# Kernel tuning notes

Hardware: AMD Instinct MI355X
Metric: run time of the kernel (lower is better)

The kernel has to match this reference:

```python
import jax, jax.numpy as jnp
import numpy as np

N_NODES = 100000
N_EDGES = 1600000
C_IN = 128
C_OUT = 128
BN_EPS = 1e-5


def setup_inputs() -> dict:
    key = jax.random.key(0)
    k = jax.random.split(key, 4)
    x = jax.random.normal(k[0], (N_NODES, C_IN), dtype=jnp.float32)
    edge_index = jax.random.randint(k[1], (2, N_EDGES), 0, N_NODES, dtype=jnp.int32)
    # nn.Linear params (Kaiming-uniform-ish scale)
    lim = 1.0 / np.sqrt(C_IN)
    W = jax.random.uniform(k[2], (C_IN, C_OUT), jnp.float32, -lim, lim)
    b = jnp.zeros((C_OUT,), jnp.float32)
    # BatchNorm (eval mode: running stats)
    gamma = jnp.ones((C_OUT,), jnp.float32)
    beta = jnp.zeros((C_OUT,), jnp.float32)
    running_mean = jnp.zeros((C_OUT,), jnp.float32)
    running_var = jnp.ones((C_OUT,), jnp.float32)
    return {"x": x, "edge_index": edge_index, "W": W, "b": b,
            "gamma": gamma, "beta": beta,
            "running_mean": running_mean, "running_var": running_var}


def reference(x, edge_index, W, b, gamma, beta, running_mean, running_var):
    # Linear projection: [N, C_in] @ [C_in, C_out]
    h = x @ W + b
    in_node, out_node = edge_index[0], edge_index[1]
    # gather edge features then scatter-mean onto destination nodes
    sums = jax.ops.segment_sum(h[in_node], out_node, num_segments=N_NODES)
    cnt = jax.ops.segment_sum(jnp.ones((in_node.shape[0],), h.dtype), out_node,
                              num_segments=N_NODES)
    agg = sums / jnp.maximum(cnt, 1.0)[:, None]  # mean; 0 for isolated nodes
    # BatchNorm1d (eval mode: running stats) + ReLU; dropout is identity in eval
    inv = jax.lax.rsqrt(running_var + BN_EPS)
    out = (agg - running_mean) * (inv * gamma) + beta
    return jax.nn.relu(out)
```

## Files before the change

### kernel.cpp

```cpp
#include <hip/hip_runtime.h>


#define NN 100000
#define NE 1600000
#define CC 128
#define BN_EPS 1e-5f
#define LBLK 1563
#define LSTR 136
#define NBUK 256
#define DPB 391
#define ACH 4096
#define ABLK 391
#define CAP 10240

typedef __attribute__((ext_vector_type(8))) short bf16x8;
typedef __attribute__((ext_vector_type(4))) float f32x4;

static __device__ __forceinline__ short f2bf(float f) {
  union { float f; unsigned u; } v; v.f = f;
  unsigned r = (v.u + 0x7FFF + ((v.u >> 16) & 1)) >> 16;
  return (short)r;
}
static __device__ __forceinline__ float bflo(unsigned p) {
  return __uint_as_float(p << 16);
}
static __device__ __forceinline__ float bfhi(unsigned p) {
  return __uint_as_float(p & 0xffff0000u);
}

__global__ __launch_bounds__(256) void prep_zero(
    const float* __restrict__ W, const float* __restrict__ bias,
    const float* __restrict__ gamma, const float* __restrict__ beta,
    const float* __restrict__ rmean, const float* __restrict__ rvar,
    short* __restrict__ Wsw, float* __restrict__ scsh,
    int* __restrict__ bhist) {
  const int i = blockIdx.x * 256 + threadIdx.x;
  if (i < NBUK) bhist[i] = 0;
  if (i < CC * CC) {
    const int k = i >> 7, n = i & 127;
    const int nt = n & 7, m = n >> 3;
    const int kb = k >> 5, q = (k >> 3) & 3, j = k & 7;
    Wsw[(size_t)(((nt * 4 + kb) * 64 + (m + 16 * q)) * 8 + j)] = f2bf(W[i]);
  }
  if (i < CC) {
    const float sc = gamma[i] * rsqrtf(rvar[i] + BN_EPS);
    scsh[i] = sc;
    scsh[CC + i] = beta[i] - rmean[i] * sc;
    scsh[2 * CC + i] = bias[i];
  }
}

__global__ __launch_bounds__(256) void bucket_hist(const int* __restrict__ ei,
                                                   int* __restrict__ bhist) {
  __shared__ int lh[NBUK];
  const int t = threadIdx.x;
  lh[t] = 0;
  __syncthreads();
  const int e0 = blockIdx.x * ACH;
  const int e1 = min(NE, e0 + ACH);
  for (int e = e0 + t; e < e1; e += 256) atomicAdd(&lh[ei[NE + e] / DPB], 1);
  __syncthreads();
  if (lh[t]) atomicAdd(&bhist[t], lh[t]);
}

__global__ __launch_bounds__(256) void bucket_scan(
    const int* __restrict__ bhist, int* __restrict__ bbase,
    int* __restrict__ gcur) {
  __shared__ int s[NBUK];
  const int t = threadIdx.x;
  const int v = bhist[t];
  s[t] = v;
  __syncthreads();
  for (int d = 1; d < 256; d <<= 1) {
    int a = (t >= d) ? s[t - d] : 0;
    __syncthreads();
    s[t] += a;
    __syncthreads();
  }
  const int ex = s[t] - v;
  bbase[t] = ex;
  gcur[t] = ex;
  if (t == 255) bbase[256] = NE;
}

__global__ __launch_bounds__(256) void bucket_scatter(
    const int* __restrict__ ei, int* __restrict__ gcur,
    int2* __restrict__ ebuf) {
  __shared__ int lh[NBUK], lbase[NBUK], lgb[NBUK], lc[NBUK];
  __shared__ int2 sorted[ACH];
  const int t = threadIdx.x;
  const int e0 = blockIdx.x * ACH;
  const int e1 = min(NE, e0 + ACH);

  lh[t] = 0;
  __syncthreads();
  for (int e = e0 + t; e < e1; e += 256) atomicAdd(&lh[ei[NE + e] / DPB], 1);
  __syncthreads();

  lbase[t] = lh[t];
  __syncthreads();
  for (int d = 1; d < 256; d <<= 1) {
    int a = (t >= d) ? lbase[t - d] : 0;
    __syncthreads();
    lbase[t] += a;
    __syncthreads();
  }
  const int excl = lbase[t] - lh[t];
  __syncthreads();
  lbase[t] = excl;
  lc[t] = excl;
  if (lh[t] > 0) lgb[t] = atomicAdd(&gcur[t], lh[t]);
  __syncthreads();

  for (int e = e0 + t; e < e1; e += 256) {
    const int src = ei[e], dst = ei[NE + e];
    const int b = dst / DPB;
    const int p = atomicAdd(&lc[b], 1);
    sorted[p] = make_int2(src, dst);
  }
  __syncthreads();

  const int n = e1 - e0;
  for (int i = t; i < n; i += 256) {
    const int2 v = sorted[i];
    const int b = v.y / DPB;
    ebuf[lgb[b] + (i - lbase[b])] = v;
  }
}

__global__ __launch_bounds__(256) void bucket_to_csr(
    const int2* __restrict__ ebuf, const int* __restrict__ bbase,
    int* __restrict__ off, int* __restrict__ csr) {
  __shared__ int dh[512];
  __shared__ int s[512];
  __shared__ int lcur[512];
  __shared__ int lcsr[CAP];
  const int b = blockIdx.x, t = threadIdx.x;
  const int lo = b * DPB;
  const int hi = min(NN, lo + DPB);
  const int nd = hi - lo;
  const int segbase = bbase[b];
  const int seglen = bbase[b + 1] - segbase;
  const int2* eb = ebuf + segbase;

  for (int i = t; i < 512; i += 256) dh[i] = 0;
  __syncthreads();
  for (int i = t; i < seglen; i += 256) atomicAdd(&dh[eb[i].y - lo], 1);
  __syncthreads();

  for (int i = t; i < 512; i += 256) s[i] = dh[i];
  __syncthreads();
  for (int d = 1; d < 512; d <<= 1) {
    const int a0 = (t >= d) ? s[t - d] : 0;
    const int a1 = (t + 256 >= d) ? s[t + 256 - d] : 0;
    __syncthreads();
    s[t] += a0;
    s[t + 256] += a1;
    __syncthreads();
  }
  for (int i = t; i < 512; i += 256) lcur[i] = s[i] - dh[i];
  for (int d = t; d < nd; d += 256) off[lo + d] = segbase + (s[d] - dh[d]);
  if (b == NBUK - 1 && t == 0) off[NN] = NE;
  __syncthreads();

  if (seglen <= CAP) {
    for (int i = t; i < seglen; i += 256) {
      const int2 e = eb[i];
      const int p = atomicAdd(&lcur[e.y - lo], 1);
      lcsr[p] = e.x;
    }
    __syncthreads();
    for (int i = t; i < seglen; i += 256) csr[segbase + i] = lcsr[i];
  } else {
    for (int i = t; i < seglen; i += 256) {
      const int2 e = eb[i];
      const int p = atomicAdd(&lcur[e.y - lo], 1);
      csr[segbase + p] = e.x;
    }
  }
}

__global__ __launch_bounds__(256) void linear_mfma(
    const float* __restrict__ x, const short* __restrict__ Wsw,
    const float* __restrict__ scsh, short* __restrict__ hout) {
  __shared__ short lsA[64 * LSTR];
  const int t = threadIdx.x;
  const int n0 = blockIdx.x * 64;

#pragma unroll
  for (int j = 0; j < 8; ++j) {
    const int idx = j * 256 + t;
    const int row = idx >> 5, kc4 = idx & 31;
    float4 v = make_float4(0.f, 0.f, 0.f, 0.f);
    if (n0 + row < NN) v = *(const float4*)(x + (size_t)(n0 + row) * CC + kc4 * 4);
    short4 sv;
    sv.x = f2bf(v.x); sv.y = f2bf(v.y); sv.z = f2bf(v.z); sv.w = f2bf(v.w);
    *(short4*)(lsA + row * LSTR + kc4 * 4) = sv;
  }
  __syncthreads();

  const int wave = t >> 6, lane = t & 63;
  const int quad = lane >> 4, m = lane & 15;
  const int rowbase = n0 + wave * 16;

  f32x4 acc[8];
#pragma unroll
  for (int nt = 0; nt < 8; ++nt) acc[nt] = (f32x4){0.f, 0.f, 0.f, 0.f};

#pragma unroll
  for (int kb = 0; kb < 4; ++kb) {
    const bf16x8 a =
        *(const bf16x8*)(lsA + (wave * 16 + m) * LSTR + kb * 32 + quad * 8);
#pragma unroll
    for (int nt = 0; nt < 8; ++nt) {
      bf16x8 bb = *(const bf16x8*)(Wsw + (size_t)(((nt * 4 + kb) * 64 + lane) * 8));
      acc[nt] = __builtin_amdgcn_mfma_f32_16x16x32_bf16(a, bb, acc[nt], 0, 0, 0);
    }
  }

  const float4 b0 = *(const float4*)(scsh + 2 * CC + m * 8);
  const float4 b1 = *(const float4*)(scsh + 2 * CC + m * 8 + 4);
  const float bv[8] = {b0.x, b0.y, b0.z, b0.w, b1.x, b1.y, b1.z, b1.w};

#pragma unroll
  for (int reg = 0; reg < 4; ++reg) {
    const int R = rowbase + quad * 4 + reg;
    if (R >= NN) continue;
    bf16x8 hv;
#pragma unroll
    for (int nt = 0; nt < 8; ++nt) hv[nt] = f2bf(acc[nt][reg] + bv[nt]);
    *(bf16x8*)(hout + (size_t)R * CC + m * 8) = hv;
  }
}

__global__ __launch_bounds__(256) void gather_bn_relu(
    const short* __restrict__ h, const int* __restrict__ off,
    const int* __restrict__ csr, const float* __restrict__ scsh,
    float* __restrict__ out) {
  const int node = (blockIdx.x * 256 + threadIdx.x) >> 6;
  const int lane = threadIdx.x & 63;
  if (node >= NN) return;
  const int s = off[node], e = off[node + 1];
  const unsigned* hb = (const unsigned*)h;

  float ax = 0.f, ay = 0.f;
  int i = s;
  for (; i + 7 < e; i += 8) {
    const int s0 = csr[i + 0], s1 = csr[i + 1], s2 = csr[i + 2], s3 = csr[i + 3];
    const int s4 = csr[i + 4], s5 = csr[i + 5], s6 = csr[i + 6], s7 = csr[i + 7];
    const unsigned p0 = hb[(size_t)s0 * 64 + lane];
    const unsigned p1 = hb[(size_t)s1 * 64 + lane];
    const unsigned p2 = hb[(size_t)s2 * 64 + lane];
    const unsigned p3 = hb[(size_t)s3 * 64 + lane];
    const unsigned p4 = hb[(size_t)s4 * 64 + lane];
    const unsigned p5 = hb[(size_t)s5 * 64 + lane];
    const unsigned p6 = hb[(size_t)s6 * 64 + lane];
    const unsigned p7 = hb[(size_t)s7 * 64 + lane];
    ax += ((bflo(p0) + bflo(p1)) + (bflo(p2) + bflo(p3))) +
          ((bflo(p4) + bflo(p5)) + (bflo(p6) + bflo(p7)));
    ay += ((bfhi(p0) + bfhi(p1)) + (bfhi(p2) + bfhi(p3))) +
          ((bfhi(p4) + bfhi(p5)) + (bfhi(p6) + bfhi(p7)));
  }
  for (; i + 3 < e; i += 4) {
    const int s0 = csr[i + 0], s1 = csr[i + 1], s2 = csr[i + 2], s3 = csr[i + 3];
    const unsigned p0 = hb[(size_t)s0 * 64 + lane];
    const unsigned p1 = hb[(size_t)s1 * 64 + lane];
    const unsigned p2 = hb[(size_t)s2 * 64 + lane];
    const unsigned p3 = hb[(size_t)s3 * 64 + lane];
    ax += (bflo(p0) + bflo(p1)) + (bflo(p2) + bflo(p3));
    ay += (bfhi(p0) + bfhi(p1)) + (bfhi(p2) + bfhi(p3));
  }
  for (; i < e; ++i) {
    const unsigned p = hb[(size_t)csr[i] * 64 + lane];
    ax += bflo(p);
    ay += bfhi(p);
  }
  const float inv = (e > s) ? 1.0f / (float)(e - s) : 0.0f;
  const float2 sc = *(const float2*)(scsh + 2 * lane);
  const float2 sh = *(const float2*)(scsh + CC + 2 * lane);
  float2 o;
  o.x = fmaxf(0.f, ax * inv * sc.x + sh.x);
  o.y = fmaxf(0.f, ay * inv * sc.y + sh.y);
  *(float2*)(out + (size_t)node * CC + lane * 2) = o;
}

__global__ __launch_bounds__(256) void edge_scatter(
    const float* __restrict__ x, const int* __restrict__ ei,
    float* __restrict__ sums, int* __restrict__ cnt) {
  int gt = blockIdx.x * 256 + threadIdx.x;
  int e = gt >> 5;
  int sub = gt & 31;
  if (e >= NE) return;
  int src = ei[e];
  int dst = ei[NE + e];
  const float4 v = *(const float4*)(x + (size_t)src * CC + sub * 4);
  float* o = sums + (size_t)dst * CC + sub * 4;
  unsafeAtomicAdd(o + 0, v.x);
  unsafeAtomicAdd(o + 1, v.y);
  unsafeAtomicAdd(o + 2, v.z);
  unsafeAtomicAdd(o + 3, v.w);
  if (sub == 0) atomicAdd(cnt + dst, 1);
}

__global__ __launch_bounds__(256) void gemm_bn_relu_fb(
    float* buf, const float* __restrict__ W, const float* __restrict__ bias,
    const float* __restrict__ gamma, const float* __restrict__ beta,
    const float* __restrict__ rmean, const float* __restrict__ rvar,
    const int* __restrict__ cnt) {
  __shared__ float xsT[CC][65];
  const int t = threadIdx.x;
  const int n0 = blockIdx.x * 64;
  for (int j = 0; j < 8; ++j) {
    int i = t + 256 * j;
    int row = i >> 5;
    int ko = (i & 31) * 4;
    float4 v = make_float4(0.f, 0.f, 0.f, 0.f);
    if (n0 + row < NN) v = *(const float4*)(buf + (size_t)(n0 + row) * CC + ko);
    xsT[ko + 0][row] = v.x;
    xsT[ko + 1][row] = v.y;
    xsT[ko + 2][row] = v.z;
    xsT[ko + 3][row] = v.w;
  }
  __syncthreads();
  const int cg = t & 31;
  const int ng8 = (t >> 5) * 8;
  float acc[8][4];
#pragma unroll
  for (int j = 0; j < 8; ++j)
#pragma unroll
    for (int c = 0; c < 4; ++c) acc[j][c] = 0.f;
#pragma unroll 8
  for (int k = 0; k < CC; ++k) {
    const float4 wv = *(const float4*)(W + k * CC + cg * 4);
#pragma unroll
    for (int j = 0; j < 8; ++j) {
      const float xv = xsT[k][ng8 + j];
      acc[j][0] = fmaf(xv, wv.x, acc[j][0]);
      acc[j][1] = fmaf(xv, wv.y, acc[j][1]);
      acc[j][2] = fmaf(xv, wv.z, acc[j][2]);
      acc[j][3] = fmaf(xv, wv.w, acc[j][3]);
    }
  }
  const float4 bb = *(const float4*)(bias + cg * 4);
  const float4 gg = *(const float4*)(gamma + cg * 4);
  const float4 bt = *(const float4*)(beta + cg * 4);
  const float4 mu = *(const float4*)(rmean + cg * 4);
  const float4 vr = *(const float4*)(rvar + cg * 4);
  float sc[4], sh[4];
  sc[0] = gg.x * rsqrtf(vr.x + BN_EPS);
  sc[1] = gg.y * rsqrtf(vr.y + BN_EPS);
  sc[2] = gg.z * rsqrtf(vr.z + BN_EPS);
  sc[3] = gg.w * rsqrtf(vr.w + BN_EPS);
  sh[0] = bt.x - mu.x * sc[0];
  sh[1] = bt.y - mu.y * sc[1];
  sh[2] = bt.z - mu.z * sc[2];
  sh[3] = bt.w - mu.w * sc[3];
#pragma unroll
  for (int j = 0; j < 8; ++j) {
    const int n = n0 + ng8 + j;
    if (n >= NN) continue;
    const int cn = cnt[n];
    const float inv = cn > 0 ? 1.0f / (float)cn : 0.0f;
    const float bsel = cn > 0 ? 1.0f : 0.0f;
    float4 o;
    o.x = fmaxf(0.f, (acc[j][0] * inv + bsel * bb.x) * sc[0] + sh[0]);
    o.y = fmaxf(0.f, (acc[j][1] * inv + bsel * bb.y) * sc[1] + sh[1]);
    o.z = fmaxf(0.f, (acc[j][2] * inv + bsel * bb.z) * sc[2] + sh[2]);
    o.w = fmaxf(0.f, (acc[j][3] * inv + bsel * bb.w) * sc[3] + sh[3]);
    *(float4*)(buf + (size_t)n * CC + cg * 4) = o;
  }
}

extern "C" void kernel_launch(void* const* d_in, const int* in_sizes, int n_in,
                              void* d_out, int out_size, void* d_ws, size_t ws_size,
                              hipStream_t stream) {
  const float* x     = (const float*)d_in[0];
  const int*   ei    = (const int*)d_in[1];
  const float* W     = (const float*)d_in[2];
  const float* bias  = (const float*)d_in[3];
  const float* gamma = (const float*)d_in[4];
  const float* beta  = (const float*)d_in[5];
  const float* rmean = (const float*)d_in[6];
  const float* rvar  = (const float*)d_in[7];
  float* out = (float*)d_out;

  const size_t OFF_B  = 0;
  const size_t BH_B   = 400128;
  const size_t BB_B   = 401152;
  const size_t GC_B   = 402304;
  const size_t CSR_B  = 802304;
  const size_t SCSH_B = 7202304;
  const size_t WSW_B  = 7204352;
  const size_t H_B    = 7237120;
  const size_t NEED   = H_B + (size_t)NN * CC * 2;

  if (ws_size >= NEED) {
    int*   off   = (int*)((char*)d_ws + OFF_B);
    int*   bhist = (int*)((char*)d_ws + BH_B);
    int*   bbase = (int*)((char*)d_ws + BB_B);
    int*   gcur  = (int*)((char*)d_ws + GC_B);
    int*   csr   = (int*)((char*)d_ws + CSR_B);
    float* scsh  = (float*)((char*)d_ws + SCSH_B);
    short* Wsw   = (short*)((char*)d_ws + WSW_B);
    short* h     = (short*)((char*)d_ws + H_B);
    int2*  ebuf  = (int2*)((char*)d_ws + H_B);

    prep_zero<<<64, 256, 0, stream>>>(W, bias, gamma, beta, rmean, rvar,
                                      Wsw, scsh, bhist);
    bucket_hist<<<ABLK, 256, 0, stream>>>(ei, bhist);
    bucket_scan<<<1, 256, 0, stream>>>(bhist, bbase, gcur);
    bucket_scatter<<<ABLK, 256, 0, stream>>>(ei, gcur, ebuf);
    bucket_to_csr<<<NBUK, 256, 0, stream>>>(ebuf, bbase, off, csr);
    linear_mfma<<<LBLK, 256, 0, stream>>>(x, Wsw, scsh, h);
    gather_bn_relu<<<(NN * 64 + 255) / 256, 256, 0, stream>>>(h, off, csr,
                                                              scsh, out);
  } else {
    int* cnt = (int*)d_ws;
    hipMemsetAsync(out, 0, (size_t)NN * CC * sizeof(float), stream);
    hipMemsetAsync(cnt, 0, (size_t)NN * sizeof(int), stream);
    edge_scatter<<<(NE * 32) / 256, 256, 0, stream>>>(x, ei, out, cnt);
    gemm_bn_relu_fb<<<(NN + 63) / 64, 256, 0, stream>>>(
        out, W, bias, gamma, beta, rmean, rvar, cnt);
  }
}
```

Before: 244.2 us.

## Merge histogram into prep, fuse bucket scatter with linear GEMM, drop scan kernel

Folds the weight/BN prep into the histogram kernel and moves the 256-entry exclusive scan into each consumer block, which removes the standalone scan and zeroing kernels. The edge bucket scatter and the MFMA linear projection now run as block ranges of one launch. They use separate workspace buffers for the edge buffer and h so the two can run concurrently. The aim is fewer launches and overlap of the edge sorting with the dense GEMM. In exchange it needs more workspace, recomputes the scan redundantly in every block, and falls back to a serialized path when workspace is small.

```diff
diff --git a/kernel.cpp b/kernel.cpp
--- a/kernel.cpp
+++ b/kernel.cpp
@@ -28,14 +28,31 @@
   return __uint_as_float(p & 0xffff0000u);
 }
 
-__global__ __launch_bounds__(256) void prep_zero(
+static __device__ __forceinline__ int excl_scan256(int* a, int t, int v) {
+  a[t] = v;
+  __syncthreads();
+  for (int d = 1; d < 256; d <<= 1) {
+    const int x = (t >= d) ? a[t - d] : 0;
+    __syncthreads();
+    a[t] += x;
+    __syncthreads();
+  }
+  const int incl = a[t];
+  __syncthreads();
+  a[t] = incl - v;
+  __syncthreads();
+  return incl - v;
+}
+
+__global__ __launch_bounds__(256) void prep_hist(
     const float* __restrict__ W, const float* __restrict__ bias,
     const float* __restrict__ gamma, const float* __restrict__ beta,
     const float* __restrict__ rmean, const float* __restrict__ rvar,
-    short* __restrict__ Wsw, float* __restrict__ scsh,
-    int* __restrict__ bhist) {
-  const int i = blockIdx.x * 256 + threadIdx.x;
-  if (i < NBUK) bhist[i] = 0;
+    const int* __restrict__ ei, short* __restrict__ Wsw,
+    float* __restrict__ scsh, int* __restrict__ bhist) {
+  __shared__ int lh[NBUK];
+  const int t = threadIdx.x;
+  const int i = blockIdx.x * 256 + t;
   if (i < CC * CC) {
     const int k = i >> 7, n = i & 127;
     const int nt = n & 7, m = n >> 3;
@@ -48,12 +65,6 @@
     scsh[CC + i] = beta[i] - rmean[i] * sc;
     scsh[2 * CC + i] = bias[i];
   }
-}
-
-__global__ __launch_bounds__(256) void bucket_hist(const int* __restrict__ ei,
-                                                   int* __restrict__ bhist) {
-  __shared__ int lh[NBUK];
-  const int t = threadIdx.x;
   lh[t] = 0;
   __syncthreads();
   const int e0 = blockIdx.x * ACH;
@@ -63,129 +74,46 @@
   if (lh[t]) atomicAdd(&bhist[t], lh[t]);
 }
 
-__global__ __launch_bounds__(256) void bucket_scan(
-    const int* __restrict__ bhist, int* __restrict__ bbase,
-    int* __restrict__ gcur) {
-  __shared__ int s[NBUK];
+__global__ __launch_bounds__(256) void scatter_linear(
+    const int* __restrict__ ei, const int* __restrict__ bhist,
+    int* __restrict__ gcurz, int2* __restrict__ ebuf,
+    const float* __restrict__ x, const short* __restrict__ Wsw,
+    const float* __restrict__ scsh, short* __restrict__ hout,
+    int scat) {
+  __shared__ int2 sorted[ACH];
+  __shared__ int gsc[NBUK], lh[NBUK], lex[NBUK], rb[NBUK], lc[NBUK];
   const int t = threadIdx.x;
-  const int v = bhist[t];
-  s[t] = v;
-  __syncthreads();
-  for (int d = 1; d < 256; d <<= 1) {
-    int a = (t >= d) ? s[t - d] : 0;
-    __syncthreads();
-    s[t] += a;
-    __syncthreads();
-  }
-  const int ex = s[t] - v;
-  bbase[t] = ex;
-  gcur[t] = ex;
-  if (t == 255) bbase[256] = NE;
-}
-
-__global__ __launch_bounds__(256) void bucket_scatter(
-    const int* __restrict__ ei, int* __restrict__ gcur,
-    int2* __restrict__ ebuf) {
-  __shared__ int lh[NBUK], lbase[NBUK], lgb[NBUK], lc[NBUK];
-  __shared__ int2 sorted[ACH];
-  const int t = threadIdx.x;
-  const int e0 = blockIdx.x * ACH;
-  const int e1 = min(NE, e0 + ACH);
-
-  lh[t] = 0;
-  __syncthreads();
-  for (int e = e0 + t; e < e1; e += 256) atomicAdd(&lh[ei[NE + e] / DPB], 1);
-  __syncthreads();
-
-  lbase[t] = lh[t];
-  __syncthreads();
-  for (int d = 1; d < 256; d <<= 1) {
-    int a = (t >= d) ? lbase[t - d] : 0;
-    __syncthreads();
-    lbase[t] += a;
-    __syncthreads();
-  }
-  const int excl = lbase[t] - lh[t];
-  __syncthreads();
-  lbase[t] = excl;
-  lc[t] = excl;
-  if (lh[t] > 0) lgb[t] = atomicAdd(&gcur[t], lh[t]);
-  __syncthreads();
-
-  for (int e = e0 + t; e < e1; e += 256) {
-    const int src = ei[e], dst = ei[NE + e];
-    const int b = dst / DPB;
-    const int p = atomicAdd(&lc[b], 1);
-    sorted[p] = make_int2(src, dst);
-  }
-  __syncthreads();
-
-  const int n = e1 - e0;
-  for (int i = t; i < n; i += 256) {
-    const int2 v = sorted[i];
-    const int b = v.y / DPB;
-    ebuf[lgb[b] + (i - lbase[b])] = v;
-  }
-}
-
-__global__ __launch_bounds__(256) void bucket_to_csr(
-    const int2* __restrict__ ebuf, const int* __restrict__ bbase,
-    int* __restrict__ off, int* __restrict__ csr) {
-  __shared__ int dh[512];
-  __shared__ int s[512];
-  __shared__ int lcur[512];
-  __shared__ int lcsr[CAP];
-  const int b = blockIdx.x, t = threadIdx.x;
-  const int lo = b * DPB;
-  const int hi = min(NN, lo + DPB);
-  const int nd = hi - lo;
-  const int segbase = bbase[b];
-  const int seglen = bbase[b + 1] - segbase;
-  const int2* eb = ebuf + segbase;
-
-  for (int i = t; i < 512; i += 256) dh[i] = 0;
-  __syncthreads();
-  for (int i = t; i < seglen; i += 256) atomicAdd(&dh[eb[i].y - lo], 1);
-  __syncthreads();
-
-  for (int i = t; i < 512; i += 256) s[i] = dh[i];
-  __syncthreads();
-  for (int d = 1; d < 512; d <<= 1) {
-    const int a0 = (t >= d) ? s[t - d] : 0;
-    const int a1 = (t + 256 >= d) ? s[t + 256 - d] : 0;
-    __syncthreads();
-    s[t] += a0;
-    s[t + 256] += a1;
-    __syncthreads();
-  }
-  for (int i = t; i < 512; i += 256) lcur[i] = s[i] - dh[i];
-  for (int d = t; d < nd; d += 256) off[lo + d] = segbase + (s[d] - dh[d]);
-  if (b == NBUK - 1 && t == 0) off[NN] = NE;
-  __syncthreads();
-
-  if (seglen <= CAP) {
-    for (int i = t; i < seglen; i += 256) {
-      const int2 e = eb[i];
-      const int p = atomicAdd(&lcur[e.y - lo], 1);
-      lcsr[p] = e.x;
-    }
-    __syncthreads();
-    for (int i = t; i < seglen; i += 256) csr[segbase + i] = lcsr[i];
-  } else {
-    for (int i = t; i < seglen; i += 256) {
-      const int2 e = eb[i];
-      const int p = atomicAdd(&lcur[e.y - lo], 1);
-      csr[segbase + p] = e.x;
-    }
-  }
-}
-
-__global__ __launch_bounds__(256) void linear_mfma(
-    const float* __restrict__ x, const short* __restrict__ Wsw,
-    const float* __restrict__ scsh, short* __restrict__ hout) {
-  __shared__ short lsA[64 * LSTR];
-  const int t = threadIdx.x;
-  const int n0 = blockIdx.x * 64;
+
+  if (blockIdx.x < scat) {
+    const int e0 = blockIdx.x * ACH;
+    const int e1 = min(NE, e0 + ACH);
+    const int gbase = excl_scan256(gsc, t, bhist[t]);
+    lh[t] = 0;
+    __syncthreads();
+    for (int e = e0 + t; e < e1; e += 256) atomicAdd(&lh[ei[NE + e] / DPB], 1);
+    __syncthreads();
+    const int vh = lh[t];
+    const int lbase = excl_scan256(lex, t, vh);
+    lc[t] = lbase;
+    if (vh > 0) rb[t] = gbase + atomicAdd(&gcurz[t], vh);
+    __syncthreads();
+    for (int e = e0 + t; e < e1; e += 256) {
+      const int src = ei[e], dst = ei[NE + e];
+      const int p = atomicAdd(&lc[dst / DPB], 1);
+      sorted[p] = make_int2(src, dst);
+    }
+    __syncthreads();
+    const int n = e1 - e0;
+    for (int i = t; i < n; i += 256) {
+      const int2 v = sorted[i];
+      const int b = v.y / DPB;
+      ebuf[rb[b] + (i - lex[b])] = v;
+    }
+    return;
+  }
+
+  short* lsA = (short*)sorted;
+  const int n0 = (blockIdx.x - scat) * 64;
 
 #pragma unroll
   for (int j = 0; j < 8; ++j) {
@@ -230,6 +158,60 @@
 #pragma unroll
     for (int nt = 0; nt < 8; ++nt) hv[nt] = f2bf(acc[nt][reg] + bv[nt]);
     *(bf16x8*)(hout + (size_t)R * CC + m * 8) = hv;
+  }
+}
+
+__global__ __launch_bounds__(256) void bucket_to_csr(
+    const int2* __restrict__ ebuf, const int* __restrict__ bhist,
+    int* __restrict__ off, int* __restrict__ csr) {
+  __shared__ int gs[NBUK];
+  __shared__ int dh[512];
+  __shared__ int s[512];
+  __shared__ int lcur[512];
+  __shared__ int lcsr[CAP];
+  const int b = blockIdx.x, t = threadIdx.x;
+  excl_scan256(gs, t, bhist[t]);
+  const int segbase = gs[b];
+  const int seglen = bhist[b];
+  const int lo = b * DPB;
+  const int hi = min(NN, lo + DPB);
+  const int nd = hi - lo;
+  const int2* eb = ebuf + segbase;
+
+  for (int i = t; i < 512; i += 256) dh[i] = 0;
+  __syncthreads();
+  for (int i = t; i < seglen; i += 256) atomicAdd(&dh[eb[i].y - lo], 1);
+  __syncthreads();
+
+  for (int i = t; i < 512; i += 256) s[i] = dh[i];
+  __syncthreads();
+  for (int d = 1; d < 512; d <<= 1) {
+    const int a0 = (t >= d) ? s[t - d] : 0;
+    const int a1 = (t + 256 >= d) ? s[t + 256 - d] : 0;
+    __syncthreads();
+    s[t] += a0;
+    s[t + 256] += a1;
+    __syncthreads();
+  }
+  for (int i = t; i < 512; i += 256) lcur[i] = s[i] - dh[i];
+  for (int d = t; d < nd; d += 256) off[lo + d] = segbase + (s[d] - dh[d]);
+  if (b == NBUK - 1 && t == 0) off[NN] = NE;
+  __syncthreads();
+
+  if (seglen <= CAP) {
+    for (int i = t; i < seglen; i += 256) {
+      const int2 e = eb[i];
+      const int p = atomicAdd(&lcur[e.y - lo], 1);
+      lcsr[p] = e.x;
+    }
+    __syncthreads();
+    for (int i = t; i < seglen; i += 256) csr[segbase + i] = lcsr[i];
+  } else {
+    for (int i = t; i < seglen; i += 256) {
+      const int2 e = eb[i];
+      const int p = atomicAdd(&lcur[e.y - lo], 1);
+      csr[segbase + p] = e.x;
+    }
   }
 }
 
@@ -386,34 +368,45 @@
 
   const size_t OFF_B  = 0;
   const size_t BH_B   = 400128;
-  const size_t BB_B   = 401152;
-  const size_t GC_B   = 402304;
+  const size_t GC_B   = 401152;
   const size_t CSR_B  = 802304;
   const size_t SCSH_B = 7202304;
   const size_t WSW_B  = 7204352;
-  const size_t H_B    = 7237120;
-  const size_t NEED   = H_B + (size_t)NN * CC * 2;
-
-  if (ws_size >= NEED) {
+  const size_t EB_B   = 7237120;
+  const size_t H1_B   = 20037120;
+  const size_t NEED1  = H1_B + (size_t)NN * CC * 2;
+  const size_t NEED2  = EB_B + (size_t)NN * CC * 2;
+
+  if (ws_size >= NEED2) {
     int*   off   = (int*)((char*)d_ws + OFF_B);
     int*   bhist = (int*)((char*)d_ws + BH_B);
-    int*   bbase = (int*)((char*)d_ws + BB_B);
-    int*   gcur  = (int*)((char*)d_ws + GC_B);
+    int*   gcurz = (int*)((char*)d_ws + GC_B);
     int*   csr   = (int*)((char*)d_ws + CSR_B);
     float* scsh  = (float*)((char*)d_ws + SCSH_B);
     short* Wsw   = (short*)((char*)d_ws + WSW_B);
-    short* h     = (short*)((char*)d_ws + H_B);
-    int2*  ebuf  = (int2*)((char*)d_ws + H_B);
-
-    prep_zero<<<64, 256, 0, stream>>>(W, bias, gamma, beta, rmean, rvar,
-                                      Wsw, scsh, bhist);
-    bucket_hist<<<ABLK, 256, 0, stream>>>(ei, bhist);
-    bucket_scan<<<1, 256, 0, stream>>>(bhist, bbase, gcur);
-    bucket_scatter<<<ABLK, 256, 0, stream>>>(ei, gcur, ebuf);
-    bucket_to_csr<<<NBUK, 256, 0, stream>>>(ebuf, bbase, off, csr);
-    linear_mfma<<<LBLK, 256, 0, stream>>>(x, Wsw, scsh, h);
-    gather_bn_relu<<<(NN * 64 + 255) / 256, 256, 0, stream>>>(h, off, csr,
-                                                              scsh, out);
+
+    hipMemsetAsync(bhist, 0, 2048, stream);
+    prep_hist<<<ABLK, 256, 0, stream>>>(W, bias, gamma, beta, rmean, rvar,
+                                        ei, Wsw, scsh, bhist);
+    if (ws_size >= NEED1) {
+      int2*  ebuf = (int2*)((char*)d_ws + EB_B);
+      short* h    = (short*)((char*)d_ws + H1_B);
+      scatter_linear<<<ABLK + LBLK, 256, 0, stream>>>(
+          ei, bhist, gcurz, ebuf, x, Wsw, scsh, h, ABLK);
+      bucket_to_csr<<<NBUK, 256, 0, stream>>>(ebuf, bhist, off, csr);
+      gather_bn_relu<<<(NN * 64 + 255) / 256, 256, 0, stream>>>(h, off, csr,
+                                                                scsh, out);
+    } else {
+      int2*  ebuf = (int2*)((char*)d_ws + EB_B);
+      short* h    = (short*)((char*)d_ws + EB_B);
+      scatter_linear<<<ABLK, 256, 0, stream>>>(
+          ei, bhist, gcurz, ebuf, x, Wsw, scsh, h, ABLK);
+      bucket_to_csr<<<NBUK, 256, 0, stream>>>(ebuf, bhist, off, csr);
+      scatter_linear<<<LBLK, 256, 0, stream>>>(
+          ei, bhist, gcurz, ebuf, x, Wsw, scsh, h, 0);
+      gather_bn_relu<<<(NN * 64 + 255) / 256, 256, 0, stream>>>(h, off, csr,
+                                                                scsh, out);
+    }
   } else {
     int* cnt = (int*)d_ws;
     hipMemsetAsync(out, 0, (size_t)NN * CC * sizeof(float), stream);
```

After: 239.2 us. 1.02x faster.
